# Kernel tuning notes

Hardware: AMD Instinct MI355X
Metric: run time of the kernel (lower is better)

The kernel has to match this reference:

```python
import jax, jax.numpy as jnp
import numpy as np

H1, H2, F1, F2 = 16, 16, 8, 1

def gcn_conv(x, src, dst, W, b, n_nodes):
    # PyG GCNConv: add self-loops (done by caller), deg-normalized mean-style aggregation
    h = x @ W  # [N, out]
    deg = jax.ops.segment_sum(jnp.ones_like(dst, dtype=h.dtype), dst, num_segments=n_nodes)
    dinv = jnp.where(deg > 0, deg ** -0.5, 0.0)
    norm = dinv[src] * dinv[dst]  # [E]
    agg = jax.ops.segment_sum(h[src] * norm[:, None], dst, num_segments=n_nodes)
    return agg + b


def setup_inputs() -> dict:
    key = jax.random.key(0)
    ks = jax.random.split(key, 12)
    N, E, G, NG = 320000, 5120000, 1000, 32
    x = jax.random.normal(ks[0], (N, 1), dtype=jnp.float32)
    edge_index = jax.random.randint(ks[1], (2, E), 0, N, dtype=jnp.int64)
    y = jax.random.normal(ks[2], (NG * G,), dtype=jnp.float32)
    gene_idx = jax.random.randint(ks[3], (1, G), 0, N // NG, dtype=jnp.int64)
    s = lambda fi, fo: (2.0 / (fi + fo)) ** 0.5
    return {
        'x': x, 'edge_index': edge_index, 'y': y, 'gene_idx': gene_idx, 'num_graphs': NG,
        'W1': jax.random.normal(ks[4], (1, H1), dtype=jnp.float32) * s(1, H1),
        'b1': jnp.zeros((H1,), dtype=jnp.float32),
        'W2': jax.random.normal(ks[5], (H1, H2), dtype=jnp.float32) * s(H1, H2),
        'b2': jnp.zeros((H2,), dtype=jnp.float32),
        'fc1_W': jax.random.normal(ks[6], (H2, F1), dtype=jnp.float32) * s(H2, F1),
        'fc1_b': jnp.zeros((F1,), dtype=jnp.float32),
        'fc2_W': jax.random.normal(ks[7], (F1, F2), dtype=jnp.float32) * s(F1, F2),
        'fc2_b': jnp.zeros((F2,), dtype=jnp.float32),
    }


def reference(x, edge_index, y, gene_idx, num_graphs, W1, b1, W2, b2, fc1_W, fc1_b, fc2_W, fc2_b):
    N = x.shape[0]
    loops = jnp.arange(N, dtype=edge_index.dtype)
    src = jnp.concatenate([edge_index[0], loops])
    dst = jnp.concatenate([edge_index[1], loops])

    h = jax.nn.relu(gcn_conv(x, src, dst, W1, b1, N))
    # F.dropout(p=0.4) is a no-op for a deterministic reference (identity at eval)
    h = jax.nn.relu(gcn_conv(h, src, dst, W2, b2, N))

    # vectorized form of the python gather loop: idx + i * nodes_per_graph, i = 0..reps-1
    nodes_per_graph = N // num_graphs
    reps = y.shape[0] // gene_idx.shape[1]
    offsets = (jnp.arange(reps, dtype=gene_idx.dtype) * nodes_per_graph)[:, None]
    all_idx = (gene_idx[0][None, :] + offsets).reshape(-1)  # [reps*G]
    t = h[all_idx]  # [reps*G, 16]

    t = jax.nn.relu(t @ fc1_W + fc1_b)
    return t @ fc2_W + fc2_b
```

## Files before the change

kernel.cpp:

```cpp
#include <hip/hip_runtime.h>


#define MAXB 17
#define RS_BITS 10
#define RS (1 << RS_BITS)
#define SRC_BITS 19
#define SRC_MASK ((1u << SRC_BITS) - 1u)
#define SENT 0xFFFFFFFFu
#define CMAX 160
#define NPGW_MAX 2048
#define BK_BT 512
#define BK_EPT 16
#define BK_TILE (BK_BT * BK_EPT)

__global__ void k_fill_f(float* __restrict__ w, float v, int n) {
    int i = blockIdx.x * blockDim.x + threadIdx.x;
    if (i < n) w[i] = v;
}
__global__ void k_fill_i(int* __restrict__ w, int v, int n) {
    int i = blockIdx.x * blockDim.x + threadIdx.x;
    if (i < n) w[i] = v;
}

__global__ void k_gprep(const float* __restrict__ W1, const float* __restrict__ b1,
                        const int* __restrict__ gene_idx,
                        float* __restrict__ bnd, int* __restrict__ prepI,
                        int* __restrict__ gmap, unsigned* __restrict__ gbit,
                        int G, int npg, int npgw) {
    int t = threadIdx.x;
    for (int i = t; i < npg; i += 256) gmap[i] = -1;
    for (int i = t; i < npgw; i += 256) gbit[i] = 0;
    __syncthreads();
    for (int g = t; g < G; g += 256) {
        int gi = gene_idx[g];
        if ((unsigned)gi < (unsigned)npg) {
            gmap[gi] = g;
            atomicOr(&gbit[gi >> 5], 1u << (gi & 31));
        }
    }
    if (t != 0) return;
    float tt[16]; int type[16]; int pos[16];
    float thr[16]; int nt = 0;
    for (int j = 0; j < 16; j++) {
        float W = W1[j], B = b1[j];
        if (W > 0.f)      { type[j] = 0; tt[j] = -B / W; }
        else if (W < 0.f) { type[j] = 1; tt[j] = -B / W; }
        else              { type[j] = (B > 0.f) ? 2 : 3; tt[j] = 0.f; }
    }
    for (int j = 0; j < 16; j++) {
        if (type[j] > 1) continue;
        float v = tt[j];
        int k = 0; while (k < nt && thr[k] < v) k++;
        if (!(k < nt && thr[k] == v)) {
            for (int m = nt; m > k; m--) thr[m] = thr[m - 1];
            thr[k] = v; nt++;
        }
    }
    int K = nt + 1;
    for (int j = 0; j < 16; j++) {
        if (type[j] <= 1) { int k = 0; while (thr[k] != tt[j]) k++; pos[j] = k; }
        else pos[j] = 0;
    }
    for (int k = 0; k < 16; k++) bnd[k] = (k < nt) ? thr[k] : 3.4e38f;
    prepI[0] = K;
    for (int k = 0; k < K; k++) {
        unsigned m = 0;
        for (int j = 0; j < 16; j++) {
            bool act;
            if (type[j] == 0)      act = (k >= pos[j] + 1);
            else if (type[j] == 1) act = (k <= pos[j]);
            else                   act = (type[j] == 2);
            if (act) m |= (1u << j);
        }
        prepI[1 + k] = (int)m;
    }
}

__global__ void k_cmap(const int* __restrict__ gmap, const unsigned* __restrict__ gbit,
                       int* __restrict__ cm, int* __restrict__ cslot, int* __restrict__ mc,
                       int N, int R, int npg, int reps, int G) {
    __shared__ int cnt;
    int r = blockIdx.x;
    if (r >= R) return;
    if (threadIdx.x == 0) cnt = 0;
    __syncthreads();
    int b0 = r << RS_BITS;
    for (int i = threadIdx.x; i < RS; i += 256) {
        int v = b0 + i;
        if (v >= N) continue;
        int rep = v / npg;
        int gi = v - rep * npg;
        int out = -1;
        if (rep < reps && ((gbit[gi >> 5] >> (gi & 31)) & 1u)) {
            int g = gmap[gi];
            if (g >= 0) {
                int sl = rep * G + g;
                int c = atomicAdd(&cnt, 1);
                if (c < CMAX) { cslot[r * CMAX + c] = sl; out = c; }
                else out = -(sl + 2);
            }
        }
        cm[v] = out;
    }
    __syncthreads();
    if (threadIdx.x == 0) mc[r] = min(cnt, CMAX);
}


__global__ void k_hist(const int* __restrict__ dst, int* __restrict__ histG,
                       int E, int N, int R) {
    __shared__ int h[512];
    for (int i = threadIdx.x; i < R; i += blockDim.x) h[i] = 0;
    __syncthreads();
    int E4 = E >> 2;
    const int4* d4 = (const int4*)dst;
    for (int e = blockIdx.x * blockDim.x + threadIdx.x; e < E4; e += gridDim.x * blockDim.x) {
        int4 d = d4[e];
        if ((unsigned)d.x < (unsigned)N) atomicAdd(&h[d.x >> RS_BITS], 1);
        if ((unsigned)d.y < (unsigned)N) atomicAdd(&h[d.y >> RS_BITS], 1);
        if ((unsigned)d.z < (unsigned)N) atomicAdd(&h[d.z >> RS_BITS], 1);
        if ((unsigned)d.w < (unsigned)N) atomicAdd(&h[d.w >> RS_BITS], 1);
    }
    for (int e = (E4 << 2) + blockIdx.x * blockDim.x + threadIdx.x; e < E;
         e += gridDim.x * blockDim.x) {
        int d = dst[e];
        if ((unsigned)d < (unsigned)N) atomicAdd(&h[d >> RS_BITS], 1);
    }
    __syncthreads();
    for (int i = threadIdx.x; i < R; i += blockDim.x) {
        int c = h[i];
        if (c) atomicAdd(&histG[i], c);
    }
}

__global__ void k_scan(const int* __restrict__ histG, int* __restrict__ base,
                       int* __restrict__ mcur, int* __restrict__ ucur, int R) {
    __shared__ int a[512];
    int t = threadIdx.x;
    int v = (t < R) ? ((histG[t] + 3) & ~3) : 0;
    a[t] = v;
    __syncthreads();
    for (int off = 1; off < 512; off <<= 1) {
        int add = (t >= off) ? a[t - off] : 0;
        __syncthreads();
        a[t] += add;
        __syncthreads();
    }
    if (t < R) { int ex = a[t] - v; base[t] = ex; mcur[t] = ex; ucur[t] = ex + v; }
}

__global__ void __launch_bounds__(BK_BT)
k_bucket(const int* __restrict__ src, const int* __restrict__ dst,
         const unsigned* __restrict__ gbit,
         int* __restrict__ mcurG, int* __restrict__ ucurG, unsigned* __restrict__ bucket,
         int E, int N, int R, int cap, int npg, int reps, int npgw) {
    __shared__ unsigned bitL[NPGW_MAX];
    __shared__ int mcnt[512], ucnt[512], mbase[512], ubase[512];
    int tile0 = blockIdx.x * BK_TILE;
    for (int i = threadIdx.x; i < npgw; i += BK_BT) bitL[i] = gbit[i];
    for (int i = threadIdx.x; i < R; i += BK_BT) { mcnt[i] = 0; ucnt[i] = 0; }
    __syncthreads();
    int ds[BK_EPT]; unsigned ss[BK_EPT];
#pragma unroll
    for (int c = 0; c < 4; c++) {
        int e0 = tile0 + c * (BK_BT * 4) + threadIdx.x * 4;
#pragma unroll
        for (int k = 0; k < 4; k++) {
            int e = e0 + k;
            int idx = c * 4 + k;
            ds[idx] = -1;
            if (e < E) {
                int d = dst[e], s = src[e];
                if ((unsigned)d < (unsigned)N && (unsigned)s < (unsigned)N) {
                    int rep = d / npg;
                    int gi = d - rep * npg;
                    unsigned m = (rep < reps && ((bitL[gi >> 5] >> (gi & 31)) & 1u)) ? 1u : 0u;
                    ds[idx] = d;
                    ss[idx] = (unsigned)s | (m << 30);
                    atomicAdd(m ? &mcnt[d >> RS_BITS] : &ucnt[d >> RS_BITS], 1);
                }
            }
        }
    }
    __syncthreads();
    for (int r = threadIdx.x; r < R; r += BK_BT) {
        int c = mcnt[r];
        mbase[r] = c > 0 ? atomicAdd(&mcurG[r], c) : 0;
        mcnt[r] = 0;
        int u = ucnt[r];
        ubase[r] = u > 0 ? (atomicSub(&ucurG[r], u) - u) : 0;
        ucnt[r] = 0;
    }
    __syncthreads();
#pragma unroll
    for (int i = 0; i < BK_EPT; i++) {
        int d = ds[i];
        if (d < 0) continue;
        int r = d >> RS_BITS;
        unsigned m = ss[i] >> 30;
        int o = atomicAdd(m ? &mcnt[r] : &ucnt[r], 1);
        int idx = (m ? mbase[r] : ubase[r]) + o;
        if ((unsigned)idx < (unsigned)cap)
            bucket[idx] = ((unsigned)(d & (RS - 1)) << SRC_BITS) | (ss[i] & SRC_MASK);
    }
}


__global__ void __launch_bounds__(1024)
k_degR2(const unsigned* __restrict__ bucket, const int* __restrict__ base,
        const int* __restrict__ histG, int* __restrict__ pDeg, int cap, int S) {
    __shared__ int degL[RS];
    int r = blockIdx.x / S, q = blockIdx.x % S;
    int nb = base[r];
    int cnt = min((histG[r] + 3) & ~3, cap - nb);
    if (cnt < 0) cnt = 0;
    int lo = (int)(((long long)cnt * q / S) & ~3LL);
    int hi = (q == S - 1) ? cnt : (int)(((long long)cnt * (q + 1) / S) & ~3LL);
    for (int i = threadIdx.x; i < RS; i += blockDim.x) degL[i] = 0;
    __syncthreads();
    for (int i = lo + threadIdx.x * 4; i < hi; i += blockDim.x * 4) {
        uint4 e4 = *(const uint4*)(bucket + nb + i);
        if (i + 0 < hi && e4.x != SENT) atomicAdd(&degL[e4.x >> SRC_BITS], 1);
        if (i + 1 < hi && e4.y != SENT) atomicAdd(&degL[e4.y >> SRC_BITS], 1);
        if (i + 2 < hi && e4.z != SENT) atomicAdd(&degL[e4.z >> SRC_BITS], 1);
        if (i + 3 < hi && e4.w != SENT) atomicAdd(&degL[e4.w >> SRC_BITS], 1);
    }
    __syncthreads();
    int* out = pDeg + (size_t)(r * S + q) * RS;
    for (int i = threadIdx.x; i < RS; i += blockDim.x) out[i] = degL[i];
}

__global__ void k_dinvp2(const int* __restrict__ pDeg, const float* __restrict__ x,
                         float* __restrict__ sd, float* __restrict__ p, int N, int S) {
    int v = blockIdx.x * blockDim.x + threadIdx.x;
    if (v >= N) return;
    int r = v >> RS_BITS, l = v & (RS - 1);
    int deg = 0;
    for (int q = 0; q < S; q++) deg += pDeg[(size_t)(r * S + q) * RS + l];
    float di = rsqrtf((float)deg + 1.0f);
    sd[2 * v + 1] = di;
    p[v] = x[v] * di;
}

__global__ void __launch_bounds__(1024)
k_t1R2(const unsigned* __restrict__ bucket, const int* __restrict__ base,
       const int* __restrict__ histG, const float* __restrict__ p,
       float* __restrict__ pT1, int cap, int S) {
    __shared__ float accL[RS];
    int r = blockIdx.x / S, q = blockIdx.x % S;
    int nb = base[r];
    int cnt = min((histG[r] + 3) & ~3, cap - nb);
    if (cnt < 0) cnt = 0;
    int lo = (int)(((long long)cnt * q / S) & ~3LL);
    int hi = (q == S - 1) ? cnt : (int)(((long long)cnt * (q + 1) / S) & ~3LL);
    for (int i = threadIdx.x; i < RS; i += blockDim.x) accL[i] = 0.f;
    __syncthreads();
    for (int i = lo + threadIdx.x * 4; i < hi; i += blockDim.x * 4) {
        uint4 e4 = *(const uint4*)(bucket + nb + i);
        if (i + 0 < hi && e4.x != SENT) atomicAdd(&accL[e4.x >> SRC_BITS], p[e4.x & SRC_MASK]);
        if (i + 1 < hi && e4.y != SENT) atomicAdd(&accL[e4.y >> SRC_BITS], p[e4.y & SRC_MASK]);
        if (i + 2 < hi && e4.z != SENT) atomicAdd(&accL[e4.z >> SRC_BITS], p[e4.z & SRC_MASK]);
        if (i + 3 < hi && e4.w != SENT) atomicAdd(&accL[e4.w >> SRC_BITS], p[e4.w & SRC_MASK]);
    }
    __syncthreads();
    float* out = pT1 + (size_t)(r * S + q) * RS;
    for (int i = threadIdx.x; i < RS; i += blockDim.x) out[i] = accL[i];
}

__global__ void k_s3(const float* __restrict__ pT1, const float* __restrict__ p,
                     float* __restrict__ sd, int N, int S) {
    int v = blockIdx.x * blockDim.x + threadIdx.x;
    if (v >= N) return;
    int r = v >> RS_BITS, l = v & (RS - 1);
    float t1 = 0.f;
    for (int q = 0; q < S; q++) t1 += pT1[(size_t)(r * S + q) * RS + l];
    sd[2 * v] = sd[2 * v + 1] * (t1 + p[v]);
}

__global__ void k_aggS(const unsigned* __restrict__ bucket, const int* __restrict__ base,
                       const int* __restrict__ mcur, const int* __restrict__ histG,
                       const float* __restrict__ sd, const int* __restrict__ cm,
                       const int* __restrict__ cslot, const int* __restrict__ mc,
                       const float* __restrict__ bnd, const int* __restrict__ prepI,
                       float* __restrict__ aggb8, int N, int cap) {
    __shared__ float acc[CMAX * 8];
    __shared__ int cmapL[RS];
    __shared__ float sB[3];
    __shared__ int sK;
    if (threadIdx.x == 0) sK = prepI[0];
    if (threadIdx.x < 3) sB[threadIdx.x] = bnd[threadIdx.x];
    __syncthreads();
    int K = sK;
    if (K > 4) return;
    int r = blockIdx.x;
    int b0 = r << RS_BITS;
    for (int i = threadIdx.x; i < RS; i += 256) {
        int v = b0 + i;
        cmapL[i] = (v < N) ? cm[v] : -1;
    }
    for (int i = threadIdx.x; i < CMAX * 8; i += 256) acc[i] = 0.f;
    __syncthreads();
    int nb = base[r];
    int pad = min((histG[r] + 3) & ~3, cap - nb);
    if (pad < 0) pad = 0;
    int mlen = mcur[r] - nb;
    if (mlen < 0) mlen = 0;
    if (mlen > pad) mlen = pad;
    const float2* sd2 = (const float2*)sd;
    for (int i = threadIdx.x * 4; i < mlen; i += 256 * 4) {
        uint4 e4 = *(const uint4*)(bucket + nb + i);
        unsigned ee[4] = {e4.x, e4.y, e4.z, e4.w};
#pragma unroll
        for (int k4 = 0; k4 < 4; k4++) {
            if (i + k4 >= mlen) break;
            unsigned e = ee[k4];
            int c = cmapL[e >> SRC_BITS];
            if (c == -1) continue;
            float2 v = sd2[e & SRC_MASK];
            int b = 0;
            for (int k = 0; k < K - 1; k++) b += (v.x > sB[k]) ? 1 : 0;
            if (c >= 0) {
                atomicAdd(&acc[c * 8 + 2 * b], v.x * v.y);
                atomicAdd(&acc[c * 8 + 2 * b + 1], v.y);
            } else {
                int sl = -(c + 2);
                atomicAdd(&aggb8[(size_t)sl * 8 + 2 * b], v.x * v.y);
                atomicAdd(&aggb8[(size_t)sl * 8 + 2 * b + 1], v.y);
            }
        }
    }
    __syncthreads();
    int mcR = mc[r];
    for (int idx = threadIdx.x; idx < mcR * 8; idx += 256) {
        int c = idx >> 3, j = idx & 7;
        int sl = cslot[r * CMAX + c];
        if (sl >= 0) aggb8[(size_t)sl * 8 + j] = acc[idx];
    }
}

__global__ void k_fillWide(const int* __restrict__ prepI, float* __restrict__ wide, int n) {
    if (prepI[0] <= 4) return;
    int i = blockIdx.x * blockDim.x + threadIdx.x;
    if (i < n) wide[i] = 0.f;
}


__global__ void k_mark(const int* __restrict__ gene_idx, int* __restrict__ slot,
                       int G, int M, int npg, int N) {
    int i = blockIdx.x * blockDim.x + threadIdx.x;
    if (i >= M) return;
    int node = gene_idx[i % G] + (i / G) * npg;
    if ((unsigned)node < (unsigned)N) slot[node] = i;
}

__global__ void k_deg(const int* __restrict__ dst, float* __restrict__ deg, int E, int N) {
    int e = blockIdx.x * blockDim.x + threadIdx.x;
    if (e >= E) return;
    int d = dst[e];
    if ((unsigned)d < (unsigned)N) atomicAdd(&deg[d], 1.0f);
}

__global__ void k_dinv_p(const float* __restrict__ x, float* __restrict__ degv,
                         float* __restrict__ p, int N) {
    int v = blockIdx.x * blockDim.x + threadIdx.x;
    if (v < N) {
        float di = rsqrtf(degv[v] + 1.0f);
        degv[v] = di;
        p[v] = x[v] * di;
    }
}

__global__ void k_scatter1(const int* __restrict__ src, const int* __restrict__ dst,
                           const float* __restrict__ p, float* __restrict__ t1, int E, int N) {
    int e = blockIdx.x * blockDim.x + threadIdx.x;
    if (e >= E) return;
    int s = src[e];
    int d = dst[e];
    if ((unsigned)s < (unsigned)N && (unsigned)d < (unsigned)N)
        atomicAdd(&t1[d], p[s]);
}

__global__ void k_s(const float* __restrict__ p, const float* __restrict__ dinv,
                    float* __restrict__ t1, int N) {
    int v = blockIdx.x * blockDim.x + threadIdx.x;
    if (v < N) t1[v] = dinv[v] * (t1[v] + p[v]);
}

__global__ void k_agg_atomic(const int* __restrict__ src, const int* __restrict__ dst,
                             const float* __restrict__ sA, const float* __restrict__ dA,
                             int str, const int* __restrict__ cm, const int* __restrict__ cslot,
                             const float* __restrict__ bnd, const int* __restrict__ prepI,
                             float* __restrict__ wide, int E, int N, int force, int mode) {
    __shared__ float sB[16];
    __shared__ int sK;
    if (threadIdx.x == 0) sK = prepI[0];
    if (threadIdx.x < 16) sB[threadIdx.x] = bnd[threadIdx.x];
    __syncthreads();
    int K = sK;
    if (!force && K <= 4) return;
    int T = K - 1;
    for (int e = blockIdx.x * blockDim.x + threadIdx.x; e < E; e += gridDim.x * blockDim.x) {
        int d = dst[e];
        if ((unsigned)d >= (unsigned)N) continue;
        int c = cm[d];
        int sl;
        if (mode == 0) sl = c;
        else sl = (c >= 0) ? cslot[(d >> RS_BITS) * CMAX + c] : (c <= -2 ? -(c + 2) : -1);
        if (sl < 0) continue;
        int sv = src[e];
        if ((unsigned)sv >= (unsigned)N) continue;
        float sval = sA[(size_t)sv * str];
        float di = dA[(size_t)sv * str];
        int b = 0;
        for (int i = 0; i < T; i++) b += (sval > sB[i]) ? 1 : 0;
        float* row = wide + (size_t)sl * (2 * MAXB) + 2 * b;
        atomicAdd(row, sval * di);
        atomicAdd(row + 1, di);
    }
}

__global__ void k_final(const float* __restrict__ aggb8, const float* __restrict__ wide,
                        const float* __restrict__ sA, const float* __restrict__ dA, int str,
                        const int* __restrict__ gene_idx, const int* __restrict__ cm,
                        const int* __restrict__ cslot, const int* __restrict__ prepI,
                        const float* __restrict__ W1, const float* __restrict__ b1,
                        const float* __restrict__ W2, const float* __restrict__ b2,
                        const float* __restrict__ f1W, const float* __restrict__ f1b,
                        const float* __restrict__ f2W, const float* __restrict__ f2b,
                        float* __restrict__ out, int G, int M, int npg, int N, int mode) {
    __shared__ float sW1[16], sb1[16], sW2[256], sb2[16], sf1[128], sf1b[8], sf2[8], sf2b[1];
    __shared__ int sMask[MAXB], sK;
    for (int i = threadIdx.x; i < 256; i += blockDim.x) sW2[i] = W2[i];
    for (int i = threadIdx.x; i < 128; i += blockDim.x) sf1[i] = f1W[i];
    if (threadIdx.x < 16) { sW1[threadIdx.x] = W1[threadIdx.x]; sb1[threadIdx.x] = b1[threadIdx.x]; sb2[threadIdx.x] = b2[threadIdx.x]; }
    if (threadIdx.x < 8)  { sf1b[threadIdx.x] = f1b[threadIdx.x]; sf2[threadIdx.x] = f2W[threadIdx.x]; }
    if (threadIdx.x == 0) { sf2b[0] = f2b[0]; sK = prepI[0]; }
    if (threadIdx.x < MAXB) sMask[threadIdx.x] = prepI[1 + threadIdx.x];
    __syncthreads();

    int i = blockIdx.x * blockDim.x + threadIdx.x;
    if (i >= M) return;
    int node = gene_idx[i % G] + (i / G) * npg;
    if ((unsigned)node >= (unsigned)N) { out[i] = 0.0f; return; }
    int K = sK;
    int c = cm[node];
    int sl;
    if (mode == 0) sl = c;
    else sl = (c >= 0) ? cslot[(node >> RS_BITS) * CMAX + c] : (c <= -2 ? -(c + 2) : -1);

    float di = dA[(size_t)node * str];
    float sval = sA[(size_t)node * str];

    float bu[MAXB], bw[MAXB];
    if (sl >= 0) {
        const float* row = (mode == 1 && K <= 4) ? (aggb8 + (size_t)sl * 8)
                                                 : (wide + (size_t)sl * (2 * MAXB));
        for (int k = 0; k < K; k++) { bu[k] = row[2 * k]; bw[k] = row[2 * k + 1]; }
    } else {
        for (int k = 0; k < K; k++) { bu[k] = 0.f; bw[k] = 0.f; }
    }

    float a[16];
#pragma unroll
    for (int j = 0; j < 16; j++) {
        float Su = 0.f, Sw = 0.f;
        for (int k = 0; k < K; k++) {
            if ((sMask[k] >> j) & 1) { Su += bu[k]; Sw += bw[k]; }
        }
        float aggj = sW1[j] * Su + sb1[j] * Sw;
        float qself = fmaxf(fmaf(sW1[j], sval, sb1[j]), 0.0f) * di;
        a[j] = di * (aggj + qself);
    }
    float h2[16];
#pragma unroll
    for (int j = 0; j < 16; j++) {
        float acc = sb2[j];
#pragma unroll
        for (int k = 0; k < 16; k++) acc = fmaf(a[k], sW2[k * 16 + j], acc);
        h2[j] = fmaxf(acc, 0.0f);
    }
    float f1[8];
#pragma unroll
    for (int j = 0; j < 8; j++) {
        float acc = sf1b[j];
#pragma unroll
        for (int k = 0; k < 16; k++) acc = fmaf(h2[k], sf1[k * 8 + j], acc);
        f1[j] = fmaxf(acc, 0.0f);
    }
    float o = sf2b[0];
#pragma unroll
    for (int k = 0; k < 8; k++) o = fmaf(f1[k], sf2[k], o);
    out[i] = o;
}

extern "C" void kernel_launch(void* const* d_in, const int* in_sizes, int n_in,
                              void* d_out, int out_size, void* d_ws, size_t ws_size,
                              hipStream_t stream) {
    const float* x        = (const float*)d_in[0];
    const int*   ei       = (const int*)d_in[1];
    const int*   gene_idx = (const int*)d_in[3];
    const float* W1  = (const float*)d_in[5];
    const float* b1  = (const float*)d_in[6];
    const float* W2  = (const float*)d_in[7];
    const float* b2  = (const float*)d_in[8];
    const float* f1W = (const float*)d_in[9];
    const float* f1b = (const float*)d_in[10];
    const float* f2W = (const float*)d_in[11];
    const float* f2b = (const float*)d_in[12];
    float* out = (float*)d_out;

    int N = in_sizes[0];
    int E = in_sizes[1] / 2;
    int M = in_sizes[2];
    int G = in_sizes[3];
    int npg = (int)(((long long)N * (long long)G) / (long long)M);
    int reps = (G > 0) ? M / G : 0;
    int npgw = (npg + 31) / 32;

    const int* src = ei;
    const int* dst = ei + E;

    int R = (N + RS - 1) >> RS_BITS;
    int cap = E + 4 * R + 4;
    const int tb = 256;

    float* ws = (float*)d_ws;
    size_t off = 0;
    float*    sd     = ws + off;              off += (size_t)2 * N;
    int*      cm     = (int*)(ws + off);      off += (size_t)N;
    float*    p      = ws + off;              off += (size_t)N;
    float*    aggb8  = ws + off;              off += (size_t)8 * M;
    unsigned* bucket = (unsigned*)(ws + off); off += (size_t)cap;
    float*    wide   = (float*)bucket;
    int*      gmap   = (int*)(ws + off);      off += (size_t)npg;
    unsigned* gbit   = (unsigned*)(ws + off); off += (size_t)npgw;
    int*      cslot  = (int*)(ws + off);      off += (size_t)R * CMAX;
    int*      mc     = (int*)(ws + off);      off += (size_t)R;
    int*      histG  = (int*)(ws + off);      off += (size_t)R;
    int*      baseA  = (int*)(ws + off);      off += (size_t)R;
    int*      mcur   = (int*)(ws + off);      off += (size_t)R;
    int*      ucur   = (int*)(ws + off);      off += (size_t)R;
    float*    bnd    = ws + off;              off += 16;
    int*      prepI  = (int*)(ws + off);      off += 20;
    size_t base_need = off;

    int S = 4;
    while (S > 1 && (base_need + (size_t)R * S * RS) * 4 > ws_size) S >>= 1;
    float* partial = ws + base_need;
    int*   partialI = (int*)partial;
    size_t need = (base_need + (size_t)R * S * RS) * 4;

    bool use_new = (need <= ws_size) && (N < (1 << SRC_BITS)) && (R <= 512) &&
                   (npg >= 1) && (npg <= NPGW_MAX * 32) && (reps >= 1) &&
                   ((size_t)cap * 4 >= (size_t)2 * MAXB * M * 4);

    if (use_new) {
        int BTr = (S == 1) ? 1024 : 256;
        k_fill_i<<<(cap + tb - 1) / tb, tb, 0, stream>>>((int*)bucket, -1, cap);
        k_fill_i<<<(R + tb - 1) / tb, tb, 0, stream>>>(histG, 0, R);
        k_gprep<<<1, 256, 0, stream>>>(W1, b1, gene_idx, bnd, prepI, gmap, gbit, G, npg, npgw);
        k_cmap<<<R, tb, 0, stream>>>(gmap, gbit, cm, cslot, mc, N, R, npg, reps, G);
        k_hist<<<512, tb, 0, stream>>>(dst, histG, E, N, R);
        k_scan<<<1, 512, 0, stream>>>(histG, baseA, mcur, ucur, R);
        int ntiles = (E + BK_TILE - 1) / BK_TILE;
        k_bucket<<<ntiles, BK_BT, 0, stream>>>(src, dst, gbit, mcur, ucur, bucket,
                                               E, N, R, cap, npg, reps, npgw);
        k_degR2<<<R * S, BTr, 0, stream>>>(bucket, baseA, histG, partialI, cap, S);
        k_dinvp2<<<(N + tb - 1) / tb, tb, 0, stream>>>(partialI, x, sd, p, N, S);
        k_t1R2<<<R * S, BTr, 0, stream>>>(bucket, baseA, histG, p, partial, cap, S);
        k_s3<<<(N + tb - 1) / tb, tb, 0, stream>>>(partial, p, sd, N, S);
        k_fill_f<<<(8 * M + tb - 1) / tb, tb, 0, stream>>>(aggb8, 0.0f, 8 * M);
        k_aggS<<<R, tb, 0, stream>>>(bucket, baseA, mcur, histG, sd, cm, cslot, mc,
                                     bnd, prepI, aggb8, N, cap);
        int wn = 2 * MAXB * M;
        k_fillWide<<<(wn + tb - 1) / tb, tb, 0, stream>>>(prepI, wide, wn);
        k_agg_atomic<<<2048, tb, 0, stream>>>(src, dst, sd, sd + 1, 2, cm, cslot, bnd,
                                              prepI, wide, E, N, 0, 1);
        k_final<<<(M + tb - 1) / tb, tb, 0, stream>>>(aggb8, wide, sd, sd + 1, 2, gene_idx,
                                                      cm, cslot, prepI, W1, b1, W2, b2,
                                                      f1W, f1b, f2W, f2b, out, G, M, npg, N,
                                                      1);
    } else {
        float* deg   = ws;
        float* t1o   = ws + (size_t)N;
        float* pO    = ws + 2 * (size_t)N;
        int*   slotO = (int*)(ws + 3 * (size_t)N);
        float* wideO = ws + 4 * (size_t)N;
        float* bndO  = wideO + (size_t)2 * MAXB * M;
        int*   prepO = (int*)(bndO + 16);

        k_fill_f<<<(2 * N + tb - 1) / tb, tb, 0, stream>>>(deg, 0.0f, 2 * N);
        k_fill_i<<<(N + tb - 1) / tb, tb, 0, stream>>>(slotO, -1, N);
        k_fill_f<<<(2 * MAXB * M + tb - 1) / tb, tb, 0, stream>>>(wideO, 0.0f, 2 * MAXB * M);
        k_gprep<<<1, 256, 0, stream>>>(W1, b1, gene_idx, bndO, prepO,
                                       (int*)wideO, (unsigned*)(wideO + npg), 0, 1, 1);
        k_mark<<<(M + tb - 1) / tb, tb, 0, stream>>>(gene_idx, slotO, G, M, npg, N);
        k_deg<<<(E + tb - 1) / tb, tb, 0, stream>>>(dst, deg, E, N);
        k_dinv_p<<<(N + tb - 1) / tb, tb, 0, stream>>>(x, deg, pO, N);
        k_scatter1<<<(E + tb - 1) / tb, tb, 0, stream>>>(src, dst, pO, t1o, E, N);
        k_s<<<(N + tb - 1) / tb, tb, 0, stream>>>(pO, deg, t1o, N);
        k_agg_atomic<<<2048, tb, 0, stream>>>(src, dst, t1o, deg, 1, slotO, (int*)0, bndO,
                                              prepO, wideO, E, N, 1, 0);
        k_final<<<(M + tb - 1) / tb, tb, 0, stream>>>((float*)0, wideO, t1o, deg, 1, gene_idx,
                                                      slotO, (int*)0, prepO, W1, b1, W2, b2,
                                                      f1W, f1b, f2W, f2b, out, G, M, npg, N,
                                                      0);
    }
}
```

Measured before the change: 267.6 us.

## Fuse cmap and histogram, drop bucket fill, pack cursors into 64-bit atomics

Merges the compute-map and dst histogram kernels into one launch, and the histogram now also counts marked edges so the scan can set exact segment bases and write sentinels only into the padding. This removes the full-bucket -1 fill. The bucket kernel now uses vectorized int4 loads, a magic-multiply division, and packed 16/16-bit shared counters with one 64-bit global atomic per region. It also folds the aggb8 zeroing into k_s3 and shrinks the grids of the fillWide and atomic-agg kernels. The magic divide assumes a bounded range of d, and the packed 16-bit counters assume per-tile counts stay below 65536.

```diff
diff --git a/kernel.cpp b/kernel.cpp
--- a/kernel.cpp
+++ b/kernel.cpp
@@ -9,9 +9,15 @@
 #define SENT 0xFFFFFFFFu
 #define CMAX 160
 #define NPGW_MAX 2048
+#define HB 512
 #define BK_BT 512
 #define BK_EPT 16
 #define BK_TILE (BK_BT * BK_EPT)
+#define PAD4(x) (((x) + 3) & ~3)
+
+__device__ __forceinline__ int div_npg(int d, unsigned long long magic) {
+    return (int)(((unsigned long long)(unsigned)d * magic) >> 45);
+}
 
 __global__ void k_fill_f(float* __restrict__ w, float v, int n) {
     int i = blockIdx.x * blockDim.x + threadIdx.x;
@@ -26,10 +32,12 @@
                         const int* __restrict__ gene_idx,
                         float* __restrict__ bnd, int* __restrict__ prepI,
                         int* __restrict__ gmap, unsigned* __restrict__ gbit,
-                        int G, int npg, int npgw) {
+                        int* __restrict__ histT, int* __restrict__ histM,
+                        int G, int npg, int npgw, int R) {
     int t = threadIdx.x;
     for (int i = t; i < npg; i += 256) gmap[i] = -1;
     for (int i = t; i < npgw; i += 256) gbit[i] = 0;
+    for (int i = t; i < R; i += 256) { histT[i] = 0; histM[i] = 0; }
     __syncthreads();
     for (int g = t; g < G; g += 256) {
         int gi = gene_idx[g];
@@ -76,69 +84,88 @@
     }
 }
 
-__global__ void k_cmap(const int* __restrict__ gmap, const unsigned* __restrict__ gbit,
-                       int* __restrict__ cm, int* __restrict__ cslot, int* __restrict__ mc,
-                       int N, int R, int npg, int reps, int G) {
-    __shared__ int cnt;
-    int r = blockIdx.x;
-    if (r >= R) return;
-    if (threadIdx.x == 0) cnt = 0;
-    __syncthreads();
-    int b0 = r << RS_BITS;
-    for (int i = threadIdx.x; i < RS; i += 256) {
-        int v = b0 + i;
-        if (v >= N) continue;
-        int rep = v / npg;
-        int gi = v - rep * npg;
-        int out = -1;
-        if (rep < reps && ((gbit[gi >> 5] >> (gi & 31)) & 1u)) {
-            int g = gmap[gi];
-            if (g >= 0) {
-                int sl = rep * G + g;
-                int c = atomicAdd(&cnt, 1);
-                if (c < CMAX) { cslot[r * CMAX + c] = sl; out = c; }
-                else out = -(sl + 2);
+__global__ void k_cmap_hist(const int* __restrict__ gmap, const unsigned* __restrict__ gbit,
+                            const int* __restrict__ dst,
+                            int* __restrict__ cm, int* __restrict__ cslot, int* __restrict__ mc,
+                            int* __restrict__ histT, int* __restrict__ histM,
+                            int N, int R, int npg, int reps, int G, int E, int npgw,
+                            unsigned long long magic) {
+    __shared__ unsigned bitL[NPGW_MAX];
+    for (int i = threadIdx.x; i < npgw; i += 256) bitL[i] = gbit[i];
+    if (blockIdx.x < (unsigned)R) {
+        __shared__ int cnt;
+        if (threadIdx.x == 0) cnt = 0;
+        __syncthreads();
+        int r = blockIdx.x;
+        int b0 = r << RS_BITS;
+        for (int i = threadIdx.x; i < RS; i += 256) {
+            int v = b0 + i;
+            if (v >= N) continue;
+            int rep = div_npg(v, magic);
+            int gi = v - rep * npg;
+            int out = -1;
+            if (rep < reps && ((bitL[gi >> 5] >> (gi & 31)) & 1u)) {
+                int g = gmap[gi];
+                if (g >= 0) {
+                    int sl = rep * G + g;
+                    int c = atomicAdd(&cnt, 1);
+                    if (c < CMAX) { cslot[r * CMAX + c] = sl; out = c; }
+                    else out = -(sl + 2);
+                }
             }
-        }
-        cm[v] = out;
-    }
-    __syncthreads();
-    if (threadIdx.x == 0) mc[r] = min(cnt, CMAX);
-}
-
-
-__global__ void k_hist(const int* __restrict__ dst, int* __restrict__ histG,
-                       int E, int N, int R) {
-    __shared__ int h[512];
-    for (int i = threadIdx.x; i < R; i += blockDim.x) h[i] = 0;
-    __syncthreads();
-    int E4 = E >> 2;
-    const int4* d4 = (const int4*)dst;
-    for (int e = blockIdx.x * blockDim.x + threadIdx.x; e < E4; e += gridDim.x * blockDim.x) {
-        int4 d = d4[e];
-        if ((unsigned)d.x < (unsigned)N) atomicAdd(&h[d.x >> RS_BITS], 1);
-        if ((unsigned)d.y < (unsigned)N) atomicAdd(&h[d.y >> RS_BITS], 1);
-        if ((unsigned)d.z < (unsigned)N) atomicAdd(&h[d.z >> RS_BITS], 1);
-        if ((unsigned)d.w < (unsigned)N) atomicAdd(&h[d.w >> RS_BITS], 1);
-    }
-    for (int e = (E4 << 2) + blockIdx.x * blockDim.x + threadIdx.x; e < E;
-         e += gridDim.x * blockDim.x) {
-        int d = dst[e];
-        if ((unsigned)d < (unsigned)N) atomicAdd(&h[d >> RS_BITS], 1);
-    }
-    __syncthreads();
-    for (int i = threadIdx.x; i < R; i += blockDim.x) {
-        int c = h[i];
-        if (c) atomicAdd(&histG[i], c);
-    }
-}
-
-__global__ void k_scan(const int* __restrict__ histG, int* __restrict__ base,
-                       int* __restrict__ mcur, int* __restrict__ ucur, int R) {
+            cm[v] = out;
+        }
+        __syncthreads();
+        if (threadIdx.x == 0) mc[r] = min(cnt, CMAX);
+    } else {
+        __shared__ int hT[512], hM[512];
+        for (int i = threadIdx.x; i < R; i += 256) { hT[i] = 0; hM[i] = 0; }
+        __syncthreads();
+        int hb = blockIdx.x - R;
+        int stride = HB * 256;
+        int E4 = E >> 2;
+        const int4* d4p = (const int4*)dst;
+        for (int e = hb * 256 + threadIdx.x; e < E4; e += stride) {
+            int4 d4 = d4p[e];
+            int dd[4] = {d4.x, d4.y, d4.z, d4.w};
+#pragma unroll
+            for (int k = 0; k < 4; k++) {
+                int d = dd[k];
+                if ((unsigned)d >= (unsigned)N) continue;
+                atomicAdd(&hT[d >> RS_BITS], 1);
+                int rep = div_npg(d, magic);
+                int gi = d - rep * npg;
+                if (rep < reps && ((bitL[gi >> 5] >> (gi & 31)) & 1u))
+                    atomicAdd(&hM[d >> RS_BITS], 1);
+            }
+        }
+        for (int e = (E4 << 2) + hb * 256 + threadIdx.x; e < E; e += stride) {
+            int d = dst[e];
+            if ((unsigned)d >= (unsigned)N) continue;
+            atomicAdd(&hT[d >> RS_BITS], 1);
+            int rep = div_npg(d, magic);
+            int gi = d - rep * npg;
+            if (rep < reps && ((bitL[gi >> 5] >> (gi & 31)) & 1u))
+                atomicAdd(&hM[d >> RS_BITS], 1);
+        }
+        __syncthreads();
+        for (int i = threadIdx.x; i < R; i += 256) {
+            if (hT[i]) atomicAdd(&histT[i], hT[i]);
+            if (hM[i]) atomicAdd(&histM[i], hM[i]);
+        }
+    }
+}
+
+__global__ void k_scan(const int* __restrict__ histT, const int* __restrict__ histM,
+                       int* __restrict__ baseA, unsigned long long* __restrict__ cur64,
+                       unsigned* __restrict__ bucket, int R, int cap) {
     __shared__ int a[512];
     int t = threadIdx.x;
-    int v = (t < R) ? ((histG[t] + 3) & ~3) : 0;
-    a[t] = v;
+    int m = (t < R) ? histM[t] : 0;
+    int tot = (t < R) ? histT[t] : 0;
+    int u = tot - m; if (u < 0) u = 0;
+    int seg = PAD4(m) + PAD4(u);
+    a[t] = seg;
     __syncthreads();
     for (int off = 1; off < 512; off <<= 1) {
         int add = (t >= off) ? a[t - off] : 0;
@@ -146,76 +173,102 @@
         a[t] += add;
         __syncthreads();
     }
-    if (t < R) { int ex = a[t] - v; base[t] = ex; mcur[t] = ex; ucur[t] = ex + v; }
+    if (t < R) {
+        int base = a[t] - seg;
+        baseA[t] = base;
+        int mstart = base, ustart = base + PAD4(m);
+        cur64[t] = (unsigned long long)(unsigned)mstart |
+                   ((unsigned long long)(unsigned)ustart << 32);
+        for (int i = m; i < PAD4(m); i++) { int ix = mstart + i; if (ix < cap) bucket[ix] = SENT; }
+        for (int i = u; i < PAD4(u); i++) { int ix = ustart + i; if (ix < cap) bucket[ix] = SENT; }
+    }
 }
 
 __global__ void __launch_bounds__(BK_BT)
 k_bucket(const int* __restrict__ src, const int* __restrict__ dst,
-         const unsigned* __restrict__ gbit,
-         int* __restrict__ mcurG, int* __restrict__ ucurG, unsigned* __restrict__ bucket,
-         int E, int N, int R, int cap, int npg, int reps, int npgw) {
+         const unsigned* __restrict__ gbit, unsigned long long* __restrict__ cur64,
+         unsigned* __restrict__ bucket, int E, int N, int R, int cap,
+         int npg, int reps, int npgw, unsigned long long magic) {
     __shared__ unsigned bitL[NPGW_MAX];
-    __shared__ int mcnt[512], ucnt[512], mbase[512], ubase[512];
+    __shared__ int cntA[512], cntB[512], mb[512], ub[512];
+    for (int i = threadIdx.x; i < npgw; i += BK_BT) bitL[i] = gbit[i];
+    for (int i = threadIdx.x; i < R; i += BK_BT) { cntA[i] = 0; cntB[i] = 0; }
+    __syncthreads();
     int tile0 = blockIdx.x * BK_TILE;
-    for (int i = threadIdx.x; i < npgw; i += BK_BT) bitL[i] = gbit[i];
-    for (int i = threadIdx.x; i < R; i += BK_BT) { mcnt[i] = 0; ucnt[i] = 0; }
-    __syncthreads();
-    int ds[BK_EPT]; unsigned ss[BK_EPT];
+    int rr[BK_EPT]; unsigned val[BK_EPT]; unsigned mbits = 0;
 #pragma unroll
     for (int c = 0; c < 4; c++) {
         int e0 = tile0 + c * (BK_BT * 4) + threadIdx.x * 4;
+        int dd[4], ss[4];
+        if (e0 + 3 < E) {
+            int4 d4 = *(const int4*)(dst + e0);
+            int4 s4 = *(const int4*)(src + e0);
+            dd[0] = d4.x; dd[1] = d4.y; dd[2] = d4.z; dd[3] = d4.w;
+            ss[0] = s4.x; ss[1] = s4.y; ss[2] = s4.z; ss[3] = s4.w;
+        } else {
+#pragma unroll
+            for (int k = 0; k < 4; k++) {
+                int e = e0 + k;
+                dd[k] = (e < E) ? dst[e] : -1;
+                ss[k] = (e < E) ? src[e] : -1;
+            }
+        }
 #pragma unroll
         for (int k = 0; k < 4; k++) {
-            int e = e0 + k;
             int idx = c * 4 + k;
-            ds[idx] = -1;
-            if (e < E) {
-                int d = dst[e], s = src[e];
-                if ((unsigned)d < (unsigned)N && (unsigned)s < (unsigned)N) {
-                    int rep = d / npg;
-                    int gi = d - rep * npg;
-                    unsigned m = (rep < reps && ((bitL[gi >> 5] >> (gi & 31)) & 1u)) ? 1u : 0u;
-                    ds[idx] = d;
-                    ss[idx] = (unsigned)s | (m << 30);
-                    atomicAdd(m ? &mcnt[d >> RS_BITS] : &ucnt[d >> RS_BITS], 1);
-                }
+            int d = dd[k];
+            rr[idx] = -1;
+            if ((unsigned)d < (unsigned)N) {
+                int rep = div_npg(d, magic);
+                int gi = d - rep * npg;
+                unsigned m = (rep < reps && ((bitL[gi >> 5] >> (gi & 31)) & 1u)) ? 1u : 0u;
+                int s = ss[k];
+                rr[idx] = d >> RS_BITS;
+                val[idx] = ((unsigned)s < (unsigned)N)
+                               ? (((unsigned)(d & (RS - 1)) << SRC_BITS) | (unsigned)s)
+                               : SENT;
+                mbits |= m << idx;
+                atomicAdd(&cntA[d >> RS_BITS], m ? 1 : (1 << 16));
             }
         }
     }
     __syncthreads();
     for (int r = threadIdx.x; r < R; r += BK_BT) {
-        int c = mcnt[r];
-        mbase[r] = c > 0 ? atomicAdd(&mcurG[r], c) : 0;
-        mcnt[r] = 0;
-        int u = ucnt[r];
-        ubase[r] = u > 0 ? (atomicSub(&ucurG[r], u) - u) : 0;
-        ucnt[r] = 0;
+        int c = cntA[r];
+        if (c) {
+            unsigned long long add = (unsigned long long)(c & 0xFFFF) |
+                                     ((unsigned long long)(unsigned)(c >> 16) << 32);
+            unsigned long long old = atomicAdd(&cur64[r], add);
+            mb[r] = (int)(old & 0xFFFFFFFFull);
+            ub[r] = (int)(old >> 32);
+        }
     }
     __syncthreads();
 #pragma unroll
     for (int i = 0; i < BK_EPT; i++) {
-        int d = ds[i];
-        if (d < 0) continue;
-        int r = d >> RS_BITS;
-        unsigned m = ss[i] >> 30;
-        int o = atomicAdd(m ? &mcnt[r] : &ucnt[r], 1);
-        int idx = (m ? mbase[r] : ubase[r]) + o;
-        if ((unsigned)idx < (unsigned)cap)
-            bucket[idx] = ((unsigned)(d & (RS - 1)) << SRC_BITS) | (ss[i] & SRC_MASK);
+        int r = rr[i];
+        if (r < 0) continue;
+        unsigned m = (mbits >> i) & 1u;
+        int o = atomicAdd(&cntB[r], m ? 1 : (1 << 16));
+        int idx = m ? (mb[r] + (o & 0xFFFF)) : (ub[r] + (o >> 16));
+        if ((unsigned)idx < (unsigned)cap) bucket[idx] = val[i];
     }
 }
 
 
 __global__ void __launch_bounds__(1024)
-k_degR2(const unsigned* __restrict__ bucket, const int* __restrict__ base,
-        const int* __restrict__ histG, int* __restrict__ pDeg, int cap, int S) {
+k_degR2(const unsigned* __restrict__ bucket, const int* __restrict__ baseA,
+        const int* __restrict__ histT, const int* __restrict__ histM,
+        int* __restrict__ pDeg, int cap, int S) {
     __shared__ int degL[RS];
     int r = blockIdx.x / S, q = blockIdx.x % S;
-    int nb = base[r];
-    int cnt = min((histG[r] + 3) & ~3, cap - nb);
-    if (cnt < 0) cnt = 0;
-    int lo = (int)(((long long)cnt * q / S) & ~3LL);
-    int hi = (q == S - 1) ? cnt : (int)(((long long)cnt * (q + 1) / S) & ~3LL);
+    int m = histM[r];
+    int u = histT[r] - m; if (u < 0) u = 0;
+    int nb = baseA[r];
+    int len = min(PAD4(m) + PAD4(u), cap - nb);
+    if (len < 0) len = 0;
+    int lo = (int)(((long long)len * q / S) & ~3LL);
+    int hi = (q == S - 1) ? len : (int)(((long long)len * (q + 1) / S) & ~3LL);
     for (int i = threadIdx.x; i < RS; i += blockDim.x) degL[i] = 0;
     __syncthreads();
     for (int i = lo + threadIdx.x * 4; i < hi; i += blockDim.x * 4) {
@@ -243,16 +296,18 @@
 }
 
 __global__ void __launch_bounds__(1024)
-k_t1R2(const unsigned* __restrict__ bucket, const int* __restrict__ base,
-       const int* __restrict__ histG, const float* __restrict__ p,
-       float* __restrict__ pT1, int cap, int S) {
+k_t1R2(const unsigned* __restrict__ bucket, const int* __restrict__ baseA,
+       const int* __restrict__ histT, const int* __restrict__ histM,
+       const float* __restrict__ p, float* __restrict__ pT1, int cap, int S) {
     __shared__ float accL[RS];
     int r = blockIdx.x / S, q = blockIdx.x % S;
-    int nb = base[r];
-    int cnt = min((histG[r] + 3) & ~3, cap - nb);
-    if (cnt < 0) cnt = 0;
-    int lo = (int)(((long long)cnt * q / S) & ~3LL);
-    int hi = (q == S - 1) ? cnt : (int)(((long long)cnt * (q + 1) / S) & ~3LL);
+    int m = histM[r];
+    int u = histT[r] - m; if (u < 0) u = 0;
+    int nb = baseA[r];
+    int len = min(PAD4(m) + PAD4(u), cap - nb);
+    if (len < 0) len = 0;
+    int lo = (int)(((long long)len * q / S) & ~3LL);
+    int hi = (q == S - 1) ? len : (int)(((long long)len * (q + 1) / S) & ~3LL);
     for (int i = threadIdx.x; i < RS; i += blockDim.x) accL[i] = 0.f;
     __syncthreads();
     for (int i = lo + threadIdx.x * 4; i < hi; i += blockDim.x * 4) {
@@ -268,8 +323,10 @@
 }
 
 __global__ void k_s3(const float* __restrict__ pT1, const float* __restrict__ p,
-                     float* __restrict__ sd, int N, int S) {
+                     float* __restrict__ sd, float* __restrict__ aggb8, int n8,
+                     int N, int S) {
     int v = blockIdx.x * blockDim.x + threadIdx.x;
+    if (v < n8) aggb8[v] = 0.f;
     if (v >= N) return;
     int r = v >> RS_BITS, l = v & (RS - 1);
     float t1 = 0.f;
@@ -277,8 +334,8 @@
     sd[2 * v] = sd[2 * v + 1] * (t1 + p[v]);
 }
 
-__global__ void k_aggS(const unsigned* __restrict__ bucket, const int* __restrict__ base,
-                       const int* __restrict__ mcur, const int* __restrict__ histG,
+__global__ void k_aggS(const unsigned* __restrict__ bucket, const int* __restrict__ baseA,
+                       const int* __restrict__ histM,
                        const float* __restrict__ sd, const int* __restrict__ cm,
                        const int* __restrict__ cslot, const int* __restrict__ mc,
                        const float* __restrict__ bnd, const int* __restrict__ prepI,
@@ -300,12 +357,9 @@
     }
     for (int i = threadIdx.x; i < CMAX * 8; i += 256) acc[i] = 0.f;
     __syncthreads();
-    int nb = base[r];
-    int pad = min((histG[r] + 3) & ~3, cap - nb);
-    if (pad < 0) pad = 0;
-    int mlen = mcur[r] - nb;
+    int nb = baseA[r];
+    int mlen = min(histM[r], cap - nb);
     if (mlen < 0) mlen = 0;
-    if (mlen > pad) mlen = pad;
     const float2* sd2 = (const float2*)sd;
     for (int i = threadIdx.x * 4; i < mlen; i += 256 * 4) {
         uint4 e4 = *(const uint4*)(bucket + nb + i);
@@ -314,6 +368,7 @@
         for (int k4 = 0; k4 < 4; k4++) {
             if (i + k4 >= mlen) break;
             unsigned e = ee[k4];
+            if (e == SENT) continue;
             int c = cmapL[e >> SRC_BITS];
             if (c == -1) continue;
             float2 v = sd2[e & SRC_MASK];
@@ -340,8 +395,8 @@
 
 __global__ void k_fillWide(const int* __restrict__ prepI, float* __restrict__ wide, int n) {
     if (prepI[0] <= 4) return;
-    int i = blockIdx.x * blockDim.x + threadIdx.x;
-    if (i < n) wide[i] = 0.f;
+    for (int i = blockIdx.x * blockDim.x + threadIdx.x; i < n; i += gridDim.x * blockDim.x)
+        wide[i] = 0.f;
 }
 
 
@@ -516,12 +571,13 @@
     int npg = (int)(((long long)N * (long long)G) / (long long)M);
     int reps = (G > 0) ? M / G : 0;
     int npgw = (npg + 31) / 32;
+    unsigned long long magic = (npg >= 1) ? (((1ULL << 45) + npg - 1) / (unsigned)npg) : 1;
 
     const int* src = ei;
     const int* dst = ei + E;
 
     int R = (N + RS - 1) >> RS_BITS;
-    int cap = E + 4 * R + 4;
+    int cap = E + 8 * R + 8;
     const int tb = 256;
 
     float* ws = (float*)d_ws;
@@ -536,10 +592,11 @@
     unsigned* gbit   = (unsigned*)(ws + off); off += (size_t)npgw;
     int*      cslot  = (int*)(ws + off);      off += (size_t)R * CMAX;
     int*      mc     = (int*)(ws + off);      off += (size_t)R;
-    int*      histG  = (int*)(ws + off);      off += (size_t)R;
+    int*      histT  = (int*)(ws + off);      off += (size_t)R;
+    int*      histM  = (int*)(ws + off);      off += (size_t)R;
     int*      baseA  = (int*)(ws + off);      off += (size_t)R;
-    int*      mcur   = (int*)(ws + off);      off += (size_t)R;
-    int*      ucur   = (int*)(ws + off);      off += (size_t)R;
+    off = (off + 1) & ~(size_t)1;
+    unsigned long long* cur64 = (unsigned long long*)(ws + off); off += (size_t)2 * R;
     float*    bnd    = ws + off;              off += 16;
     int*      prepI  = (int*)(ws + off);      off += 20;
     size_t base_need = off;
@@ -556,26 +613,27 @@
 
     if (use_new) {
         int BTr = (S == 1) ? 1024 : 256;
-        k_fill_i<<<(cap + tb - 1) / tb, tb, 0, stream>>>((int*)bucket, -1, cap);
-        k_fill_i<<<(R + tb - 1) / tb, tb, 0, stream>>>(histG, 0, R);
-        k_gprep<<<1, 256, 0, stream>>>(W1, b1, gene_idx, bnd, prepI, gmap, gbit, G, npg, npgw);
-        k_cmap<<<R, tb, 0, stream>>>(gmap, gbit, cm, cslot, mc, N, R, npg, reps, G);
-        k_hist<<<512, tb, 0, stream>>>(dst, histG, E, N, R);
-        k_scan<<<1, 512, 0, stream>>>(histG, baseA, mcur, ucur, R);
+        k_gprep<<<1, 256, 0, stream>>>(W1, b1, gene_idx, bnd, prepI, gmap, gbit,
+                                       histT, histM, G, npg, npgw, R);
+        k_cmap_hist<<<R + HB, 256, 0, stream>>>(gmap, gbit, dst, cm, cslot, mc,
+                                                histT, histM, N, R, npg, reps, G, E,
+                                                npgw, magic);
+        k_scan<<<1, 512, 0, stream>>>(histT, histM, baseA, cur64, bucket, R, cap);
         int ntiles = (E + BK_TILE - 1) / BK_TILE;
-        k_bucket<<<ntiles, BK_BT, 0, stream>>>(src, dst, gbit, mcur, ucur, bucket,
-                                               E, N, R, cap, npg, reps, npgw);
-        k_degR2<<<R * S, BTr, 0, stream>>>(bucket, baseA, histG, partialI, cap, S);
+        k_bucket<<<ntiles, BK_BT, 0, stream>>>(src, dst, gbit, cur64, bucket,
+                                               E, N, R, cap, npg, reps, npgw, magic);
+        k_degR2<<<R * S, BTr, 0, stream>>>(bucket, baseA, histT, histM, partialI, cap, S);
         k_dinvp2<<<(N + tb - 1) / tb, tb, 0, stream>>>(partialI, x, sd, p, N, S);
-        k_t1R2<<<R * S, BTr, 0, stream>>>(bucket, baseA, histG, p, partial, cap, S);
-        k_s3<<<(N + tb - 1) / tb, tb, 0, stream>>>(partial, p, sd, N, S);
-        k_fill_f<<<(8 * M + tb - 1) / tb, tb, 0, stream>>>(aggb8, 0.0f, 8 * M);
-        k_aggS<<<R, tb, 0, stream>>>(bucket, baseA, mcur, histG, sd, cm, cslot, mc,
+        k_t1R2<<<R * S, BTr, 0, stream>>>(bucket, baseA, histT, histM, p, partial, cap, S);
+        int n8 = 8 * M;
+        int s3grid = ((N > n8 ? N : n8) + tb - 1) / tb;
+        k_s3<<<s3grid, tb, 0, stream>>>(partial, p, sd, aggb8, n8, N, S);
+        k_aggS<<<R, tb, 0, stream>>>(bucket, baseA, histM, sd, cm, cslot, mc,
                                      bnd, prepI, aggb8, N, cap);
         int wn = 2 * MAXB * M;
-        k_fillWide<<<(wn + tb - 1) / tb, tb, 0, stream>>>(prepI, wide, wn);
-        k_agg_atomic<<<2048, tb, 0, stream>>>(src, dst, sd, sd + 1, 2, cm, cslot, bnd,
-                                              prepI, wide, E, N, 0, 1);
+        k_fillWide<<<512, tb, 0, stream>>>(prepI, wide, wn);
+        k_agg_atomic<<<512, tb, 0, stream>>>(src, dst, sd, sd + 1, 2, cm, cslot, bnd,
+                                             prepI, wide, E, N, 0, 1);
         k_final<<<(M + tb - 1) / tb, tb, 0, stream>>>(aggb8, wide, sd, sd + 1, 2, gene_idx,
                                                       cm, cslot, prepI, W1, b1, W2, b2,
                                                       f1W, f1b, f2W, f2b, out, G, M, npg, N,
@@ -588,12 +646,14 @@
         float* wideO = ws + 4 * (size_t)N;
         float* bndO  = wideO + (size_t)2 * MAXB * M;
         int*   prepO = (int*)(bndO + 16);
+        int*   scr   = prepO + 20;
 
         k_fill_f<<<(2 * N + tb - 1) / tb, tb, 0, stream>>>(deg, 0.0f, 2 * N);
         k_fill_i<<<(N + tb - 1) / tb, tb, 0, stream>>>(slotO, -1, N);
         k_fill_f<<<(2 * MAXB * M + tb - 1) / tb, tb, 0, stream>>>(wideO, 0.0f, 2 * MAXB * M);
         k_gprep<<<1, 256, 0, stream>>>(W1, b1, gene_idx, bndO, prepO,
-                                       (int*)wideO, (unsigned*)(wideO + npg), 0, 1, 1);
+                                       scr, (unsigned*)(scr + 1), scr + 2, scr + 3,
+                                       0, 1, 1, 0);
         k_mark<<<(M + tb - 1) / tb, tb, 0, stream>>>(gene_idx, slotO, G, M, npg, N);
         k_deg<<<(E + tb - 1) / tb, tb, 0, stream>>>(dst, deg, E, N);
         k_dinv_p<<<(N + tb - 1) / tb, tb, 0, stream>>>(x, deg, pO, N);
```

Result: faster. 253.6 us (-5.2%).
